# Kernel tuning notes

Measured on AMD Instinct MI355X. Metric: run time of the kernel, lower is better.

The kernel has to match this reference:

```python
import jax, jax.numpy as jnp
import numpy as np

EPS = 1e-10


def setup_inputs() -> dict:
    key = jax.random.key(0)
    k1, k2, k3, k4, k5, k6 = jax.random.split(key, 6)
    N, F_IN, F_OUT, R = 200000, 128, 128, 16
    B, S = 4096, 10  # batch of target nodes, sampled neighbors per node
    emb = jax.random.normal(k1, (N, F_IN), dtype=jnp.float32)
    w_self = jax.random.normal(k2, (F_OUT, F_IN), dtype=jnp.float32) * 0.05
    w_rel = jax.random.normal(k3, (R, F_OUT, F_IN), dtype=jnp.float32) * 0.05
    nodes = jax.random.randint(k4, (B,), 0, N, dtype=jnp.int32)
    neighbors = jax.random.randint(k5, (B, S), 0, N, dtype=jnp.int32)
    rel_mask = jax.random.randint(k6, (B, S, R), 0, 2, dtype=jnp.int32)
    return {"emb": emb, "w_self": w_self, "w_rel": w_rel,
            "nodes": nodes, "neighbors": neighbors, "rel_mask": rel_mask}


def reference(emb, w_self, w_rel, nodes, neighbors, rel_mask):
    # Self term: x @ W_self^T
    x = emb[nodes]                                   # [B, Fin]  (gather)
    out = x @ w_self.T                               # [B, Fout]
    # Gather sampled neighbor embeddings
    ne = emb[neighbors]                              # [B, S, Fin] (irregular gather)
    m = rel_mask.astype(emb.dtype)                   # [B, S, R] binary relation masks
    # Per-relation masked sum over sampled neighbors
    sums = jnp.einsum('bsr,bsf->rbf', m, ne)         # [R, B, Fin]
    counts = jnp.transpose(m.sum(axis=1))[..., None] # [R, B, 1] neighbors per (rel,node)
    agg = sums / (counts + EPS)                      # masked mean (matches mask/= n+1e-10)
    # Per-relation weight matmul, summed into output
    out = out + jnp.einsum('rbf,rof->bo', agg, w_rel)
    return jax.nn.relu(out)
```

## Files before the change

kernel.cpp:

```cpp
#include <hip/hip_runtime.h>
#include <hip/hip_bf16.h>


#define BT   16
#define LDA  2184
#define NTHR 1024

typedef __attribute__((ext_vector_type(8))) short short8;
typedef __attribute__((ext_vector_type(4))) float f32x4;

__device__ __forceinline__ unsigned int pk2_rne(float lo, float hi) {
  unsigned int r;
  asm("v_cvt_pk_bf16_f32 %0, %1, %2" : "=v"(r) : "v"(lo), "v"(hi));
  return r;
}

__device__ __forceinline__ void barrier_lgkm() {
  __builtin_amdgcn_sched_barrier(0);
  asm volatile("s_waitcnt lgkmcnt(0)" ::: "memory");
  __builtin_amdgcn_s_barrier();
  __builtin_amdgcn_sched_barrier(0);
}

__global__ __launch_bounds__(256)
void wprep(const float* __restrict__ w_self, const float* __restrict__ w_rel,
           uint4* __restrict__ w2)
{
  const int u  = blockIdx.x * 4 + (threadIdx.x >> 6);
  const int l  = threadIdx.x & 63;
  const int ln = l & 15, lj = l >> 4;
  const int ks = u >> 3, ot = u & 7;
  const int o  = ot * 16 + ln;
  const int k0 = ks * 32 + lj * 8;
  const float* src;
  if (k0 < 128) src = w_self + o * 128 + k0;
  else {
    const int r = (k0 - 128) >> 7, kc = (k0 - 128) & 127;
    src = w_rel + ((size_t)(r * 128 + o)) * 128 + kc;
  }
  const float4 a = *(const float4*)src;
  const float4 b = *(const float4*)(src + 4);
  uint4 v;
  v.x = pk2_rne(a.x, a.y); v.y = pk2_rne(a.z, a.w);
  v.z = pk2_rne(b.x, b.y); v.w = pk2_rne(b.z, b.w);
  w2[u * 64 + l] = v;
}

__global__ __launch_bounds__(NTHR)
void rgcn_fused(const float* __restrict__ emb,
                const int*   __restrict__ nodes,
                const int*   __restrict__ neighbors,
                const int*   __restrict__ rel_mask,
                const uint4* __restrict__ w2,
                float*       __restrict__ out)
{
  __shared__ alignas(16) char smem[80128];
  unsigned short* A_t = (unsigned short*)smem;
  float* P = (float*)smem;
  float (*mscale)[10][16] = (float (*)[10][16])(smem + 69888);

  const int t  = threadIdx.x;
  const int l  = t & 63;
  const int w  = t >> 6;
  const int b0 = blockIdx.x * BT;

  const int og  = w & 3,  kq = w >> 2;
  const int ot0 = og * 2;
  const int ksq = kq * 17;

  const int bi   = w;
  const int b    = b0 + bi;
  const int node = nodes[b];
  int nb[10];
  {
    const int2* np = (const int2*)(neighbors + (size_t)b * 10);
    const int2 p0 = np[0], p1 = np[1], p2 = np[2], p3 = np[3], p4 = np[4];
    nb[0]=p0.x; nb[1]=p0.y; nb[2]=p1.x; nb[3]=p1.y; nb[4]=p2.x;
    nb[5]=p2.y; nb[6]=p3.x; nb[7]=p3.y; nb[8]=p4.x; nb[9]=p4.y;
  }

  int mb[10];
  if (t < 256) {
    const int* mp = rel_mask + (size_t)(b0 + (t >> 4)) * 160 + (t & 15);
    #pragma unroll
    for (int s = 0; s < 10; ++s) mb[s] = mp[s * 16];
  }

  const uint4* wq = w2 + (size_t)((ksq * 8 + ot0) * 64) + l;
  uint4 c0 = wq[0];
  uint4 c1 = wq[64];
  wq += 512;

  const int f0 = l * 2;
  float2 ne[10];
  #pragma unroll
  for (int s = 0; s < 10; ++s)
    ne[s] = *(const float2*)(emb + (size_t)nb[s] * 128 + f0);
  const float2 x2 = *(const float2*)(emb + (size_t)node * 128 + f0);

  if (t < 256) {
    int c = 0;
    #pragma unroll
    for (int s = 0; s < 10; ++s) c += mb[s];
    const float inv = 1.0f / ((float)c + 1e-10f);
    #pragma unroll
    for (int s = 0; s < 10; ++s) mscale[t >> 4][s][t & 15] = mb[s] ? inv : 0.0f;
  }
  barrier_lgkm();

  {
    char* arow = (char*)A_t + bi * (LDA * 2);
    *(unsigned int*)(arow + f0 * 2) = pk2_rne(x2.x, x2.y);
    float acc[16][2];
    #pragma unroll
    for (int r = 0; r < 16; ++r) { acc[r][0] = 0.f; acc[r][1] = 0.f; }
    #pragma unroll
    for (int s = 0; s < 10; ++s) {
      const float4 m0 = *(const float4*)(&mscale[bi][s][0]);
      const float4 m1 = *(const float4*)(&mscale[bi][s][4]);
      const float4 m2 = *(const float4*)(&mscale[bi][s][8]);
      const float4 m3 = *(const float4*)(&mscale[bi][s][12]);
      const float m[16] = {m0.x,m0.y,m0.z,m0.w, m1.x,m1.y,m1.z,m1.w,
                           m2.x,m2.y,m2.z,m2.w, m3.x,m3.y,m3.z,m3.w};
      const float2 v = ne[s];
      #pragma unroll
      for (int r = 0; r < 16; ++r) {
        acc[r][0] += m[r] * v.x;
        acc[r][1] += m[r] * v.y;
      }
    }
    #pragma unroll
    for (int r = 0; r < 16; ++r)
      *(unsigned int*)(arow + 256 + r * 256 + f0 * 2) = pk2_rne(acc[r][0], acc[r][1]);
  }
  barrier_lgkm();

  const int ln = l & 15, lj = l >> 4;
  f32x4 accA = {0.f,0.f,0.f,0.f}, accB = {0.f,0.f,0.f,0.f};
  {
    const char* ar = (const char*)A_t + ln * (LDA * 2) + lj * 16;
    #pragma unroll
    for (int i = 0; i < 17; ++i) {
      const short8 a = *(const short8*)(ar + (ksq + i) * 64);
      const uint4 n0 = wq[0];
      const uint4 n1 = wq[64];
      wq += 512;
      union { uint4 u; short8 s; } u0, u1;
      u0.u = c0; u1.u = c1;
      accA = __builtin_amdgcn_mfma_f32_16x16x32_bf16(a, u0.s, accA, 0, 0, 0);
      accB = __builtin_amdgcn_mfma_f32_16x16x32_bf16(a, u1.s, accB, 0, 0, 0);
      c0 = n0; c1 = n1;
    }
  }
  barrier_lgkm();

  {
    float* Pg = P + (kq >> 1) * 2112;
    if ((kq & 1) == 0) {
      #pragma unroll
      for (int j = 0; j < 4; ++j) {
        Pg[(lj*4+j)*132 + ot0*16 + ln]       = accA[j];
        Pg[(lj*4+j)*132 + (ot0+1)*16 + ln]   = accB[j];
      }
    }
    barrier_lgkm();
    if ((kq & 1) == 1) {
      #pragma unroll
      for (int j = 0; j < 4; ++j) {
        Pg[(lj*4+j)*132 + ot0*16 + ln]      += accA[j];
        Pg[(lj*4+j)*132 + (ot0+1)*16 + ln]  += accB[j];
      }
    }
    barrier_lgkm();
  }

  {
    const int row = w;
    const int cc  = (t & 63) * 2;
    const float2 pa = *(const float2*)(P + row * 132 + cc);
    const float2 pb = *(const float2*)(P + 2112 + row * 132 + cc);
    float2 o2;
    o2.x = fmaxf(pa.x + pb.x, 0.f);
    o2.y = fmaxf(pa.y + pb.y, 0.f);
    *(float2*)(out + (size_t)(b0 + row) * 128 + cc) = o2;
  }
}

extern "C" void kernel_launch(void* const* d_in, const int* in_sizes, int n_in,
                              void* d_out, int out_size, void* d_ws, size_t ws_size,
                              hipStream_t stream) {
  const float* emb       = (const float*)d_in[0];
  const float* w_self    = (const float*)d_in[1];
  const float* w_rel     = (const float*)d_in[2];
  const int*   nodes     = (const int*)d_in[3];
  const int*   neighbors = (const int*)d_in[4];
  const int*   rel_mask  = (const int*)d_in[5];
  float* out = (float*)d_out;
  (void)in_sizes; (void)n_in; (void)out_size; (void)ws_size;

  wprep<<<136, 256, 0, stream>>>(w_self, w_rel, (uint4*)d_ws);
  rgcn_fused<<<4096 / BT, NTHR, 0, stream>>>(
      emb, nodes, neighbors, rel_mask, (const uint4*)d_ws, out);
}
```

Measured before the change: 20.97 us.

## Fuse weight bf16 conversion into main kernel, dropping the wprep launch

Removes the separate wprep kernel that packed the fp32 weights into a bf16 MFMA-ready workspace. The fused kernel now reads fp32 w_self/w_rel directly in its MFMA loop and converts them to bf16 in registers. This saves one kernel launch and the write and re-read of the workspace. In exchange each of the 256 blocks reads twice the weight bytes (fp32 instead of bf16) from L2 and repeats the conversion work, and the loop loses the software-prefetched next-iteration loads.

```diff
diff --git a/kernel.cpp b/kernel.cpp
--- a/kernel.cpp
+++ b/kernel.cpp
@@ -22,36 +22,13 @@
   __builtin_amdgcn_sched_barrier(0);
 }
 
-__global__ __launch_bounds__(256)
-void wprep(const float* __restrict__ w_self, const float* __restrict__ w_rel,
-           uint4* __restrict__ w2)
-{
-  const int u  = blockIdx.x * 4 + (threadIdx.x >> 6);
-  const int l  = threadIdx.x & 63;
-  const int ln = l & 15, lj = l >> 4;
-  const int ks = u >> 3, ot = u & 7;
-  const int o  = ot * 16 + ln;
-  const int k0 = ks * 32 + lj * 8;
-  const float* src;
-  if (k0 < 128) src = w_self + o * 128 + k0;
-  else {
-    const int r = (k0 - 128) >> 7, kc = (k0 - 128) & 127;
-    src = w_rel + ((size_t)(r * 128 + o)) * 128 + kc;
-  }
-  const float4 a = *(const float4*)src;
-  const float4 b = *(const float4*)(src + 4);
-  uint4 v;
-  v.x = pk2_rne(a.x, a.y); v.y = pk2_rne(a.z, a.w);
-  v.z = pk2_rne(b.x, b.y); v.w = pk2_rne(b.z, b.w);
-  w2[u * 64 + l] = v;
-}
-
 __global__ __launch_bounds__(NTHR)
 void rgcn_fused(const float* __restrict__ emb,
+                const float* __restrict__ w_self,
+                const float* __restrict__ w_rel,
                 const int*   __restrict__ nodes,
                 const int*   __restrict__ neighbors,
                 const int*   __restrict__ rel_mask,
-                const uint4* __restrict__ w2,
                 float*       __restrict__ out)
 {
   __shared__ alignas(16) char smem[80128];
@@ -67,6 +44,9 @@
   const int og  = w & 3,  kq = w >> 2;
   const int ot0 = og * 2;
   const int ksq = kq * 17;
+  const int ln  = l & 15, lj = l >> 4;
+  const int o0c = ot0 * 16 + ln;
+  const int o1c = o0c + 16;
 
   const int bi   = w;
   const int b    = b0 + bi;
@@ -86,10 +66,21 @@
     for (int s = 0; s < 10; ++s) mb[s] = mp[s * 16];
   }
 
-  const uint4* wq = w2 + (size_t)((ksq * 8 + ot0) * 64) + l;
-  uint4 c0 = wq[0];
-  uint4 c1 = wq[64];
-  wq += 512;
+  float4 W0a, W0b, W1a, W1b;
+  {
+    const int k0 = ksq * 32 + lj * 8;
+    const float *p0, *p1;
+    if (k0 < 128) {
+      p0 = w_self + o0c * 128 + k0;
+      p1 = w_self + o1c * 128 + k0;
+    } else {
+      const int r = (k0 - 128) >> 7, kc = (k0 - 128) & 127;
+      p0 = w_rel + (size_t)r * 16384 + o0c * 128 + kc;
+      p1 = w_rel + (size_t)r * 16384 + o1c * 128 + kc;
+    }
+    W0a = *(const float4*)p0; W0b = *(const float4*)(p0 + 4);
+    W1a = *(const float4*)p1; W1b = *(const float4*)(p1 + 4);
+  }
 
   const int f0 = l * 2;
   float2 ne[10];
@@ -135,21 +126,37 @@
   }
   barrier_lgkm();
 
-  const int ln = l & 15, lj = l >> 4;
   f32x4 accA = {0.f,0.f,0.f,0.f}, accB = {0.f,0.f,0.f,0.f};
   {
     const char* ar = (const char*)A_t + ln * (LDA * 2) + lj * 16;
     #pragma unroll
     for (int i = 0; i < 17; ++i) {
-      const short8 a = *(const short8*)(ar + (ksq + i) * 64);
-      const uint4 n0 = wq[0];
-      const uint4 n1 = wq[64];
-      wq += 512;
-      union { uint4 u; short8 s; } u0, u1;
-      u0.u = c0; u1.u = c1;
+      const int ks = ksq + i;
+      float4 a0, a1, b0v, b1v;
+      if (i == 0) {
+        a0 = W0a; a1 = W0b; b0v = W1a; b1v = W1b;
+      } else {
+        const int k0 = ks * 32 + lj * 8;
+        const float *p0, *p1;
+        if (k0 < 128) {
+          p0 = w_self + o0c * 128 + k0;
+          p1 = w_self + o1c * 128 + k0;
+        } else {
+          const int r = (k0 - 128) >> 7, kc = (k0 - 128) & 127;
+          p0 = w_rel + (size_t)r * 16384 + o0c * 128 + kc;
+          p1 = w_rel + (size_t)r * 16384 + o1c * 128 + kc;
+        }
+        a0  = *(const float4*)p0; a1  = *(const float4*)(p0 + 4);
+        b0v = *(const float4*)p1; b1v = *(const float4*)(p1 + 4);
+      }
+      const short8 a = *(const short8*)(ar + ks * 64);
+      union { unsigned int u[4]; short8 s; } u0, u1;
+      u0.u[0] = pk2_rne(a0.x, a0.y);   u0.u[1] = pk2_rne(a0.z, a0.w);
+      u0.u[2] = pk2_rne(a1.x, a1.y);   u0.u[3] = pk2_rne(a1.z, a1.w);
+      u1.u[0] = pk2_rne(b0v.x, b0v.y); u1.u[1] = pk2_rne(b0v.z, b0v.w);
+      u1.u[2] = pk2_rne(b1v.x, b1v.y); u1.u[3] = pk2_rne(b1v.z, b1v.w);
       accA = __builtin_amdgcn_mfma_f32_16x16x32_bf16(a, u0.s, accA, 0, 0, 0);
       accB = __builtin_amdgcn_mfma_f32_16x16x32_bf16(a, u1.s, accB, 0, 0, 0);
-      c0 = n0; c1 = n1;
     }
   }
   barrier_lgkm();
@@ -159,16 +166,16 @@
     if ((kq & 1) == 0) {
       #pragma unroll
       for (int j = 0; j < 4; ++j) {
-        Pg[(lj*4+j)*132 + ot0*16 + ln]       = accA[j];
-        Pg[(lj*4+j)*132 + (ot0+1)*16 + ln]   = accB[j];
+        Pg[(lj*4+j)*132 + o0c] = accA[j];
+        Pg[(lj*4+j)*132 + o1c] = accB[j];
       }
     }
     barrier_lgkm();
     if ((kq & 1) == 1) {
       #pragma unroll
       for (int j = 0; j < 4; ++j) {
-        Pg[(lj*4+j)*132 + ot0*16 + ln]      += accA[j];
-        Pg[(lj*4+j)*132 + (ot0+1)*16 + ln]  += accB[j];
+        Pg[(lj*4+j)*132 + o0c] += accA[j];
+        Pg[(lj*4+j)*132 + o1c] += accB[j];
       }
     }
     barrier_lgkm();
@@ -176,7 +183,7 @@
 
   {
     const int row = w;
-    const int cc  = (t & 63) * 2;
+    const int cc  = l * 2;
     const float2 pa = *(const float2*)(P + row * 132 + cc);
     const float2 pb = *(const float2*)(P + 2112 + row * 132 + cc);
     float2 o2;
@@ -196,9 +203,8 @@
   const int*   neighbors = (const int*)d_in[4];
   const int*   rel_mask  = (const int*)d_in[5];
   float* out = (float*)d_out;
-  (void)in_sizes; (void)n_in; (void)out_size; (void)ws_size;
-
-  wprep<<<136, 256, 0, stream>>>(w_self, w_rel, (uint4*)d_ws);
+  (void)in_sizes; (void)n_in; (void)out_size; (void)d_ws; (void)ws_size;
+
   rgcn_fused<<<4096 / BT, NTHR, 0, stream>>>(
-      emb, nodes, neighbors, rel_mask, (const uint4*)d_ws, out);
-}
+      emb, w_self, w_rel, nodes, neighbors, rel_mask, out);
+}
```

New measurement: 40.34 us. 1.92x slower.

## Merge weight prep into main kernel using cooperative launch and grid sync

Applied to the files above, without the earlier changes.

Removes the separate weight-conversion kernel launch. The first 34 blocks convert weights to bf16 while every block gathers embeddings and builds its A tile, and a grid-wide sync then precedes the MFMA phase. This hides the weight prep behind the gather and saves one launch. In exchange it adds a grid barrier and needs all 256 blocks of 1024 threads with about 80KB LDS to be co-resident, which the 256 CUs of MI355X should allow.

```diff
diff --git a/kernel.cpp b/kernel.cpp
--- a/kernel.cpp
+++ b/kernel.cpp
@@ -1,6 +1,9 @@
 #include <hip/hip_runtime.h>
 #include <hip/hip_bf16.h>
-
+#include <hip/hip_cooperative_groups.h>
+
+
+namespace cg = cooperative_groups;
 
 #define BT   16
 #define LDA  2184
@@ -22,51 +25,53 @@
   __builtin_amdgcn_sched_barrier(0);
 }
 
-__global__ __launch_bounds__(256)
-void wprep(const float* __restrict__ w_self, const float* __restrict__ w_rel,
-           uint4* __restrict__ w2)
-{
-  const int u  = blockIdx.x * 4 + (threadIdx.x >> 6);
-  const int l  = threadIdx.x & 63;
-  const int ln = l & 15, lj = l >> 4;
-  const int ks = u >> 3, ot = u & 7;
-  const int o  = ot * 16 + ln;
-  const int k0 = ks * 32 + lj * 8;
-  const float* src;
-  if (k0 < 128) src = w_self + o * 128 + k0;
-  else {
-    const int r = (k0 - 128) >> 7, kc = (k0 - 128) & 127;
-    src = w_rel + ((size_t)(r * 128 + o)) * 128 + kc;
-  }
-  const float4 a = *(const float4*)src;
-  const float4 b = *(const float4*)(src + 4);
-  uint4 v;
-  v.x = pk2_rne(a.x, a.y); v.y = pk2_rne(a.z, a.w);
-  v.z = pk2_rne(b.x, b.y); v.w = pk2_rne(b.z, b.w);
-  w2[u * 64 + l] = v;
-}
-
 __global__ __launch_bounds__(NTHR)
-void rgcn_fused(const float* __restrict__ emb,
-                const int*   __restrict__ nodes,
-                const int*   __restrict__ neighbors,
-                const int*   __restrict__ rel_mask,
-                const uint4* __restrict__ w2,
-                float*       __restrict__ out)
+void rgcn_coop(const float* __restrict__ emb,
+               const float* __restrict__ w_self,
+               const float* __restrict__ w_rel,
+               const int*   __restrict__ nodes,
+               const int*   __restrict__ neighbors,
+               const int*   __restrict__ rel_mask,
+               uint4*       w2,
+               float*       __restrict__ out)
 {
   __shared__ alignas(16) char smem[80128];
   unsigned short* A_t = (unsigned short*)smem;
   float* P = (float*)smem;
   float (*mscale)[10][16] = (float (*)[10][16])(smem + 69888);
 
-  const int t  = threadIdx.x;
-  const int l  = t & 63;
-  const int w  = t >> 6;
-  const int b0 = blockIdx.x * BT;
+  const int t   = threadIdx.x;
+  const int l   = t & 63;
+  const int w   = t >> 6;
+  const int bid = blockIdx.x;
+  const int b0  = bid * BT;
 
   const int og  = w & 3,  kq = w >> 2;
   const int ot0 = og * 2;
   const int ksq = kq * 17;
+  const int ln  = l & 15, lj = l >> 4;
+  const int o0c = ot0 * 16 + ln;
+  const int o1c = o0c + 16;
+
+  if (bid < 34) {
+    const int u  = bid * 16 + w;
+    const int ks = u >> 3, ot = u & 7;
+    const int o  = ot * 16 + ln;
+    const int k0 = ks * 32 + lj * 8;
+    const float* src;
+    if (k0 < 128) src = w_self + o * 128 + k0;
+    else {
+      const int r = (k0 - 128) >> 7, kc = (k0 - 128) & 127;
+      src = w_rel + ((size_t)(r * 128 + o)) * 128 + kc;
+    }
+    const float4 a = *(const float4*)src;
+    const float4 b = *(const float4*)(src + 4);
+    uint4 v;
+    v.x = pk2_rne(a.x, a.y); v.y = pk2_rne(a.z, a.w);
+    v.z = pk2_rne(b.x, b.y); v.w = pk2_rne(b.z, b.w);
+    w2[u * 64 + l] = v;
+    __threadfence();
+  }
 
   const int bi   = w;
   const int b    = b0 + bi;
@@ -85,11 +90,6 @@
     #pragma unroll
     for (int s = 0; s < 10; ++s) mb[s] = mp[s * 16];
   }
-
-  const uint4* wq = w2 + (size_t)((ksq * 8 + ot0) * 64) + l;
-  uint4 c0 = wq[0];
-  uint4 c1 = wq[64];
-  wq += 512;
 
   const int f0 = l * 2;
   float2 ne[10];
@@ -135,9 +135,14 @@
   }
   barrier_lgkm();
 
-  const int ln = l & 15, lj = l >> 4;
+  cg::this_grid().sync();
+
   f32x4 accA = {0.f,0.f,0.f,0.f}, accB = {0.f,0.f,0.f,0.f};
   {
+    const uint4* wq = w2 + (size_t)((ksq * 8 + ot0) * 64) + l;
+    uint4 c0 = wq[0];
+    uint4 c1 = wq[64];
+    wq += 512;
     const char* ar = (const char*)A_t + ln * (LDA * 2) + lj * 16;
     #pragma unroll
     for (int i = 0; i < 17; ++i) {
@@ -159,16 +164,16 @@
     if ((kq & 1) == 0) {
       #pragma unroll
       for (int j = 0; j < 4; ++j) {
-        Pg[(lj*4+j)*132 + ot0*16 + ln]       = accA[j];
-        Pg[(lj*4+j)*132 + (ot0+1)*16 + ln]   = accB[j];
+        Pg[(lj*4+j)*132 + o0c] = accA[j];
+        Pg[(lj*4+j)*132 + o1c] = accB[j];
       }
     }
     barrier_lgkm();
     if ((kq & 1) == 1) {
       #pragma unroll
       for (int j = 0; j < 4; ++j) {
-        Pg[(lj*4+j)*132 + ot0*16 + ln]      += accA[j];
-        Pg[(lj*4+j)*132 + (ot0+1)*16 + ln]  += accB[j];
+        Pg[(lj*4+j)*132 + o0c] += accA[j];
+        Pg[(lj*4+j)*132 + o1c] += accB[j];
       }
     }
     barrier_lgkm();
@@ -176,7 +181,7 @@
 
   {
     const int row = w;
-    const int cc  = (t & 63) * 2;
+    const int cc  = l * 2;
     const float2 pa = *(const float2*)(P + row * 132 + cc);
     const float2 pb = *(const float2*)(P + 2112 + row * 132 + cc);
     float2 o2;
@@ -196,9 +201,11 @@
   const int*   neighbors = (const int*)d_in[4];
   const int*   rel_mask  = (const int*)d_in[5];
   float* out = (float*)d_out;
+  uint4* w2  = (uint4*)d_ws;
   (void)in_sizes; (void)n_in; (void)out_size; (void)ws_size;
 
-  wprep<<<136, 256, 0, stream>>>(w_self, w_rel, (uint4*)d_ws);
-  rgcn_fused<<<4096 / BT, NTHR, 0, stream>>>(
-      emb, nodes, neighbors, rel_mask, (const uint4*)d_ws, out);
-}
+  void* args[] = { (void*)&emb, (void*)&w_self, (void*)&w_rel, (void*)&nodes,
+                   (void*)&neighbors, (void*)&rel_mask, (void*)&w2, (void*)&out };
+  hipLaunchCooperativeKernel((const void*)rgcn_coop, dim3(4096 / BT), dim3(NTHR),
+                             args, 0, stream);
+}
```

After: 79.41 us. 3.79x slower.
